# Performance work log

Measured on AMD Instinct MI355X. Metric: run time of the kernel, lower is better.

The kernel has to match this reference:

```python
import jax, jax.numpy as jnp
import numpy as np

NUM_HEADS = 8
LN_EPS = 1e-5


def _layernorm(t, w, b):
    mu = t.mean(-1, keepdims=True)
    var = t.var(-1, keepdims=True)  # ddof=0, matches torch LayerNorm
    return (t - mu) * jax.lax.rsqrt(var + LN_EPS) * w + b


def setup_inputs() -> dict:
    key = jax.random.key(0)
    ks = jax.random.split(key, 5)
    B, C, H, W = 16, 384, 32, 32
    hidden = 4 * C
    s = 0.02
    return {
        "x": jax.random.normal(ks[0], (B, C, H, W), jnp.float32),
        "ln1_w": jnp.ones((C,), jnp.float32),
        "ln1_b": jnp.zeros((C,), jnp.float32),
        "qkv_w": s * jax.random.normal(ks[1], (3 * C, C), jnp.float32),
        "qkv_b": jnp.zeros((3 * C,), jnp.float32),
        "proj_w": s * jax.random.normal(ks[2], (C, C), jnp.float32),
        "proj_b": jnp.zeros((C,), jnp.float32),
        "ln2_w": jnp.ones((C,), jnp.float32),
        "ln2_b": jnp.zeros((C,), jnp.float32),
        "fc1_w": s * jax.random.normal(ks[3], (hidden, C), jnp.float32),
        "fc1_b": jnp.zeros((hidden,), jnp.float32),
        "fc2_w": s * jax.random.normal(ks[4], (C, hidden), jnp.float32),
        "fc2_b": jnp.zeros((C,), jnp.float32),
    }


def reference(x, ln1_w, ln1_b, qkv_w, qkv_b, proj_w, proj_b,
              ln2_w, ln2_b, fc1_w, fc1_b, fc2_w, fc2_b):
    B, C, H, W = x.shape
    N = H * W
    nh = NUM_HEADS
    hd = C // nh
    scale = hd ** (-0.5)

    xf = x.reshape(B, C, N).transpose(0, 2, 1)  # (B, N, C) tokens

    # --- pre-norm attention ---
    h1 = _layernorm(xf, ln1_w, ln1_b)
    qkv = h1 @ qkv_w.T + qkv_b                      # (B, N, 3C)
    qkv = qkv.reshape(B, N, 3, nh, hd).transpose(2, 0, 3, 1, 4)  # (3,B,h,N,d)
    q, k, v = qkv[0], qkv[1], qkv[2]
    attn = jax.nn.softmax(jnp.einsum('bhnd,bhmd->bhnm', q, k) * scale, axis=-1)
    out = jnp.einsum('bhnm,bhmd->bhnd', attn, v)    # (B,h,N,d)
    out = out.transpose(0, 2, 1, 3).reshape(B, N, C)
    out = out @ proj_w.T + proj_b
    xf = xf + out

    # --- pre-norm FFN (exact GELU, matching torch nn.GELU default) ---
    h2 = _layernorm(xf, ln2_w, ln2_b)
    f = jax.nn.gelu(h2 @ fc1_w.T + fc1_b, approximate=False)
    f = f @ fc2_w.T + fc2_b
    xf = xf + f

    return xf.transpose(0, 2, 1).reshape(B, C, H, W)
```

## Files before the change

kernel.cpp:

```cpp
#include <hip/hip_runtime.h>

typedef unsigned short u16;
using bf16x8 = __attribute__((ext_vector_type(8))) short;
using f32x4  = __attribute__((ext_vector_type(4))) float;
using f32x16 = __attribute__((ext_vector_type(16))) float;

#define DEV __device__ __forceinline__

constexpr int    NTOK = 16384;
constexpr size_t QKSZ = (size_t)16 * 8 * 1024 * 64;
constexpr float  ATTN_SCALE = 0.14433756729740645f;

DEV u16 f2bf(float x) {
  unsigned int u = __float_as_uint(x);
  u += 0x7fffu + ((u >> 16) & 1u);
  return (u16)(u >> 16);
}

DEV void async16(const u16* g, u16* l) {
  __builtin_amdgcn_global_load_lds(
      (const __attribute__((address_space(1))) unsigned int*)g,
      (__attribute__((address_space(3))) unsigned int*)l, 16, 0, 0);
}

DEV const bf16x8* lds_swz(const u16* base, int row, int bytecol) {
  int byte = row * 128 + bytecol;
  byte ^= (row & 7) << 4;
  return (const bf16x8*)((const char*)base + byte);
}

DEV f32x16 zero16() {
  f32x16 z;
#pragma unroll
  for (int i = 0; i < 16; ++i) z[i] = 0.f;
  return z;
}

DEV float gelu_f(float x) {
  float y = 0.7978845608028654f * (x + 0.044715f * x * x * x);
  float e = __expf(2.f * y);
  float t = 1.f - 2.f / (e + 1.f);
  return 0.5f * x * (1.f + t);
}

DEV void xcd_remap(int& bx, int& by) {
  int p = blockIdx.x + gridDim.x * blockIdx.y;
  int nxs = gridDim.x >> 3;
  int xcd = p & 7, q = p >> 3;
  bx = xcd * nxs + q % nxs;
  by = q / nxs;
}

__global__ void cvt_kernel(const float* __restrict__ qkvw, const float* __restrict__ qkvb,
                           const float* __restrict__ projw, const float* __restrict__ fc1w,
                           const float* __restrict__ fc2w,
                           u16* __restrict__ wqkvp, float* __restrict__ biasp,
                           u16* __restrict__ wproj, u16* __restrict__ wfc1,
                           u16* __restrict__ wfc2) {
  int i = blockIdx.x * 256 + threadIdx.x;
  if (i < 147456) {
    int p = i / 96, q = (i - p * 96) * 4;
    int which = p >> 9, h = (p >> 6) & 7, d = p & 63;
    ushort4 o{0, 0, 0, 0};
    if (d < 48) {
      float sc = which ? 1.f : ATTN_SCALE;
      float4 v = *(const float4*)(qkvw + (size_t)(which * 384 + h * 48 + d) * 384 + q);
      o = ushort4{f2bf(v.x * sc), f2bf(v.y * sc), f2bf(v.z * sc), f2bf(v.w * sc)};
    }
    *(ushort4*)(wqkvp + (size_t)p * 384 + q) = o;
  } else if (i < 479232) {
    const float* s; u16* d; int off;
    if (i < 184320)      { s = projw; d = wproj; off = i - 147456; }
    else if (i < 331776) { s = fc1w;  d = wfc1;  off = i - 184320; }
    else                 { s = fc2w;  d = wfc2;  off = i - 331776; }
    float4 v = *(const float4*)(s + (size_t)off * 4);
    *(ushort4*)(d + (size_t)off * 4) = ushort4{f2bf(v.x), f2bf(v.y), f2bf(v.z), f2bf(v.w)};
  } else if (i < 479616) {
    int qi = (i - 479232) * 4;
    float4 o;
    float* op = (float*)&o;
#pragma unroll
    for (int r = 0; r < 4; ++r) {
      int p = qi + r, which = p >> 9, h = (p >> 6) & 7, d = p & 63;
      op[r] = (d < 48) ? qkvb[which * 384 + h * 48 + d] * (which ? 1.f : ATTN_SCALE) : 0.f;
    }
    *(float4*)(biasp + qi) = o;
  }
}

__global__ __launch_bounds__(256) void ln_kernel(
    const float* __restrict__ in, const float* __restrict__ gw,
    const float* __restrict__ gb, u16* __restrict__ out) {
  __shared__ float tile[32][385];
  __shared__ float mu_s[32], rs_s[32];
  const int b = blockIdx.y;
  const int n0 = blockIdx.x * 32;
  const int t = threadIdx.x;
  const int j = t & 31, cb = t >> 5;
  const float* src = in + (size_t)b * 384 * 1024 + n0;
  for (int k = 0; k < 48; ++k) {
    int c = k * 8 + cb;
    tile[j][c] = src[(size_t)c * 1024 + j];
  }
  __syncthreads();
  const int jt = t >> 3, r = t & 7;
  float s = 0.f, ss = 0.f;
  for (int c = r; c < 384; c += 8) { float v = tile[jt][c]; s += v; ss += v * v; }
  s += __shfl_xor(s, 1); ss += __shfl_xor(ss, 1);
  s += __shfl_xor(s, 2); ss += __shfl_xor(ss, 2);
  s += __shfl_xor(s, 4); ss += __shfl_xor(ss, 4);
  const float mean = s * (1.f / 384.f);
  const float var  = ss * (1.f / 384.f) - mean * mean;
  if (r == 0) { mu_s[jt] = mean; rs_s[jt] = rsqrtf(var + 1e-5f); }
  __syncthreads();
  for (int q = t; q < 3072; q += 256) {
    int tok = q / 96, c4 = (q - tok * 96) * 4;
    float m = mu_s[tok], rv = rs_s[tok];
    float4 wv = *(const float4*)(gw + c4);
    float4 bv = *(const float4*)(gb + c4);
    u16* dst = out + (size_t)(b * 1024 + n0 + tok) * 384 + c4;
    ushort4 o{f2bf((tile[tok][c4 + 0] - m) * rv * wv.x + bv.x),
              f2bf((tile[tok][c4 + 1] - m) * rv * wv.y + bv.y),
              f2bf((tile[tok][c4 + 2] - m) * rv * wv.z + bv.z),
              f2bf((tile[tok][c4 + 3] - m) * rv * wv.w + bv.w)};
    *(ushort4*)dst = o;
  }
}

template<int EPI>
__global__ __launch_bounds__(512, 2) void gemm256_kernel(
    const u16* __restrict__ A, const u16* __restrict__ W,
    const float* __restrict__ bias, u16* __restrict__ outh, int K) {
  __shared__ u16 sA[2][8192], sB[2][8192];
  int bx, by; xcd_remap(bx, by);
  const int m0 = bx * 256, n0 = by * 256;
  const int tid = threadIdx.x;
  const int wv = tid >> 6, lane = tid & 63;
  const int wm = (wv >> 2) * 128, wn = (wv & 3) * 64;
  const int l16 = lane & 15, lg = lane >> 4;
  const int rsw = ((lg ^ (l16 & 3)) << 4);

  f32x4 acc[8][4];
#pragma unroll
  for (int i = 0; i < 8; ++i)
#pragma unroll
    for (int jj = 0; jj < 4; ++jj) acc[i][jj] = f32x4{0.f, 0.f, 0.f, 0.f};

  const int nk = K >> 5;
  auto stage = [&](int buf, int kt) {
    const u16* Ab = A + (size_t)m0 * K + kt * 32;
    const u16* Wb = W + (size_t)n0 * K + kt * 32;
#pragma unroll
    for (int j = 0; j < 2; ++j) {
      int cb = j * 512 + wv * 64;
      int c = cb + lane;
      int row = c >> 2, sl = (c & 3) ^ (row & 3);
      async16(Ab + (size_t)row * K + sl * 8, &sA[buf][cb * 8]);
      async16(Wb + (size_t)row * K + sl * 8, &sB[buf][cb * 8]);
    }
  };
  stage(0, 0);
  int buf = 0;
  for (int kt = 0; kt < nk; ++kt) {
    asm volatile("s_waitcnt vmcnt(0)" ::: "memory");
    __builtin_amdgcn_s_barrier();
    if (kt + 1 < nk) stage(buf ^ 1, kt + 1);
    bf16x8 av[8], bv[4];
#pragma unroll
    for (int f = 0; f < 4; ++f)
      bv[f] = *(const bf16x8*)((const char*)&sB[buf][0] + (wn + f * 16 + l16) * 64 + rsw);
#pragma unroll
    for (int f = 0; f < 8; ++f)
      av[f] = *(const bf16x8*)((const char*)&sA[buf][0] + (wm + f * 16 + l16) * 64 + rsw);
    __builtin_amdgcn_s_setprio(1);
#pragma unroll
    for (int mf = 0; mf < 8; ++mf)
#pragma unroll
      for (int nf = 0; nf < 4; ++nf)
        acc[mf][nf] = __builtin_amdgcn_mfma_f32_16x16x32_bf16(bv[nf], av[mf], acc[mf][nf], 0, 0, 0);
    __builtin_amdgcn_s_setprio(0);
    buf ^= 1;
  }

#pragma unroll
  for (int mf = 0; mf < 8; ++mf) {
    const int token = m0 + wm + mf * 16 + l16;
    const int b = token >> 10, nn = token & 1023;
#pragma unroll
    for (int nf = 0; nf < 4; ++nf) {
      const int col = n0 + wn + nf * 16 + lg * 4;
      f32x4 v = acc[mf][nf];
      float4 bb = *(const float4*)(bias + col);
      unsigned long long pk = 0;
      if constexpr (EPI == 0) {
#pragma unroll
        for (int rr = 0; rr < 4; ++rr)
          pk |= (unsigned long long)f2bf(v[rr] + ((const float*)&bb)[rr]) << (16 * rr);
        const int which = col >> 9, h = (col >> 6) & 7, d0 = col & 63;
        size_t idx = (size_t)which * QKSZ + (size_t)((b * 8 + h) * 1024 + nn) * 64 + d0;
        *(unsigned long long*)&outh[idx] = pk;
      } else {
#pragma unroll
        for (int rr = 0; rr < 4; ++rr)
          pk |= (unsigned long long)f2bf(gelu_f(v[rr] + ((const float*)&bb)[rr])) << (16 * rr);
        *(unsigned long long*)&outh[(size_t)token * 1536 + col] = pk;
      }
    }
  }
}

template<int EPI>
__global__ __launch_bounds__(256, 2) void gemm_kernel(
    const u16* __restrict__ A, const u16* __restrict__ W,
    const float* __restrict__ bias, float* __restrict__ outf,
    u16* __restrict__ outh, const float* __restrict__ resid, int K) {
  __shared__ u16 sA[2][8192], sB[2][8192];
  int bx, by; xcd_remap(bx, by);
  const int m0 = bx * 128;
  const int n0 = (EPI == 4 ? 1024 : 0) + by * 128;
  const int wv = threadIdx.x >> 6, lane = threadIdx.x & 63;
  const int wm = (wv >> 1) * 64, wn = (wv & 1) * 64;
  const int l16 = lane & 15, lg = lane >> 4;
  const int ksw = (l16 & 7) << 4;

  f32x4 acc[4][4];
#pragma unroll
  for (int i = 0; i < 4; ++i)
#pragma unroll
    for (int jj = 0; jj < 4; ++jj) acc[i][jj] = f32x4{0.f, 0.f, 0.f, 0.f};

  const int nk = K >> 6;
  auto stage = [&](int buf, int kt) {
    const u16* Ab = A + (size_t)m0 * K + kt * 64;
    const u16* Wb = W + (size_t)n0 * K + kt * 64;
#pragma unroll
    for (int j = 0; j < 4; ++j) {
      int cb = j * 256 + wv * 64;
      int c = cb + lane;
      int row = c >> 3, sl = (c & 7) ^ (row & 7);
      async16(Ab + (size_t)row * K + sl * 8, &sA[buf][cb * 8]);
      async16(Wb + (size_t)row * K + sl * 8, &sB[buf][cb * 8]);
    }
  };
  stage(0, 0);
  int buf = 0;
  for (int kt = 0; kt < nk; ++kt) {
    asm volatile("s_waitcnt vmcnt(0)" ::: "memory");
    __builtin_amdgcn_s_barrier();
    if (kt + 1 < nk) stage(buf ^ 1, kt + 1);
#pragma unroll
    for (int ks = 0; ks < 2; ++ks) {
      bf16x8 av[4], bv[4];
#pragma unroll
      for (int f = 0; f < 4; ++f) {
        int ra = wm + f * 16 + l16, rb = wn + f * 16 + l16;
        av[f] = *(const bf16x8*)((const char*)&sA[buf][0] + ra * 128 + ((ks * 64 + lg * 16) ^ ksw));
        bv[f] = *(const bf16x8*)((const char*)&sB[buf][0] + rb * 128 + ((ks * 64 + lg * 16) ^ ksw));
      }
      __builtin_amdgcn_s_setprio(1);
#pragma unroll
      for (int mf = 0; mf < 4; ++mf)
#pragma unroll
        for (int nf = 0; nf < 4; ++nf)
          acc[mf][nf] = __builtin_amdgcn_mfma_f32_16x16x32_bf16(av[mf], bv[nf], acc[mf][nf], 0, 0, 0);
      __builtin_amdgcn_s_setprio(0);
    }
    buf ^= 1;
  }

#pragma unroll
  for (int mf = 0; mf < 4; ++mf) {
    const int mm = m0 + wm + mf * 16 + lg * 4;
    const int b = mm >> 10, nn = mm & 1023;
#pragma unroll
    for (int nf = 0; nf < 4; ++nf) {
      const int col = n0 + wn + nf * 16 + l16;
      f32x4 v = acc[mf][nf];
      const float bs = bias[col];
      if constexpr (EPI == 4) {
        unsigned long long pk = 0;
#pragma unroll
        for (int rr = 0; rr < 4; ++rr)
          pk |= (unsigned long long)f2bf(v[rr] + bs) << (16 * rr);
        const int h = (col >> 6) & 7, d = col & 63;
        size_t idx = 2ull * QKSZ + (((size_t)((b * 8 + h) * 64 + d)) << 10) + nn;
        *(unsigned long long*)&outh[idx] = pk;
      } else {
        size_t idx = ((size_t)(b * 384 + col) << 10) + nn;
        float4 rr4 = *(const float4*)&resid[idx];
        float4 o{v[0] + bs + rr4.x, v[1] + bs + rr4.y, v[2] + bs + rr4.z, v[3] + bs + rr4.w};
        *(float4*)&outf[idx] = o;
      }
    }
  }
}

__global__ __launch_bounds__(256, 3) void attn_kernel(
    const u16* __restrict__ Qg, const u16* __restrict__ Kg,
    const u16* __restrict__ Vtg, u16* __restrict__ outp) {
  __shared__ u16 Ks[2][4096];
  __shared__ u16 Vs[2][4096];
  __shared__ u16 Qs[8192];
  const int orig = blockIdx.x;
  const int swz = (orig & 7) * 128 + (orig >> 3);
  const int bh = swz >> 3, qt = swz & 7;
  const int w = threadIdx.x >> 6, lane = threadIdx.x & 63;
  const int l31 = lane & 31, hi = lane >> 5;

  const u16* kbase = Kg + (size_t)bh * 65536;
  const u16* vbase = Vtg + (size_t)bh * 65536;

  auto stageKV = [&](int buf, int kv) {
#pragma unroll
    for (int i = 0; i < 2; ++i) {
      int cb = (i * 4 + w) * 64;
      int ck = cb + lane;
      int g  = ck ^ ((ck >> 3) & 7);
      async16(kbase + (size_t)kv * 4096 + g * 8, &Ks[buf][cb * 8]);
      async16(vbase + (size_t)(g >> 3) * 1024 + kv * 64 + (g & 7) * 8, &Vs[buf][cb * 8]);
    }
  };

  {
    const u16* src = Qg + (size_t)(bh * 1024 + qt * 128) * 64;
#pragma unroll
    for (int i = 0; i < 4; ++i) {
      int cb = (i * 4 + w) * 64;
      int ck = cb + lane;
      int g  = ck ^ ((ck >> 3) & 7);
      async16(src + g * 8, &Qs[cb * 8]);
    }
  }
  stageKV(0, 0);
  asm volatile("s_waitcnt vmcnt(0)" ::: "memory");
  __builtin_amdgcn_s_barrier();

  bf16x8 qf[4];
#pragma unroll
  for (int ds = 0; ds < 4; ++ds)
    qf[ds] = *lds_swz(Qs, w * 32 + l31, ds * 32 + hi * 16);

  f32x16 out0 = zero16(), out1 = zero16();
  float ls0 = 0.f, ls1 = 0.f;

  int buf = 0;
  for (int kv = 0; kv < 16; ++kv) {
    if (kv + 1 < 16) stageKV(buf ^ 1, kv + 1);

    f32x16 sacc0 = zero16(), sacc1 = zero16();
    __builtin_amdgcn_s_setprio(1);
#pragma unroll
    for (int ds = 0; ds < 4; ++ds) {
      bf16x8 kf0 = *lds_swz(Ks[buf], l31,      ds * 32 + hi * 16);
      bf16x8 kf1 = *lds_swz(Ks[buf], 32 + l31, ds * 32 + hi * 16);
      sacc0 = __builtin_amdgcn_mfma_f32_32x32x16_bf16(kf0, qf[ds], sacc0, 0, 0, 0);
      sacc1 = __builtin_amdgcn_mfma_f32_32x32x16_bf16(kf1, qf[ds], sacc1, 0, 0, 0);
    }
    __builtin_amdgcn_s_setprio(0);

    unsigned int c0[8], c1[8];
#pragma unroll
    for (int i = 0; i < 8; ++i) {
      float a = __expf(sacc0[2 * i]), b = __expf(sacc0[2 * i + 1]);
      ls0 += a + b;
      unsigned int pk;
      asm("v_cvt_pk_bf16_f32 %0, %1, %2" : "=v"(pk) : "v"(a), "v"(b));
      c0[i] = pk;
    }
#pragma unroll
    for (int i = 0; i < 8; ++i) {
      float a = __expf(sacc1[2 * i]), b = __expf(sacc1[2 * i + 1]);
      ls1 += a + b;
      unsigned int pk;
      asm("v_cvt_pk_bf16_f32 %0, %1, %2" : "=v"(pk) : "v"(a), "v"(b));
      c1[i] = pk;
    }

#pragma unroll
    for (int m = 0; m < 4; ++m) {
      unsigned int a0 = (m < 2) ? c0[(m & 1) * 4 + 0] : c1[(m & 1) * 4 + 0];
      unsigned int b0 = (m < 2) ? c0[(m & 1) * 4 + 2] : c1[(m & 1) * 4 + 2];
      unsigned int a1 = (m < 2) ? c0[(m & 1) * 4 + 1] : c1[(m & 1) * 4 + 1];
      unsigned int b1 = (m < 2) ? c0[(m & 1) * 4 + 3] : c1[(m & 1) * 4 + 3];
      asm volatile("v_permlane32_swap_b32 %0, %1" : "+v"(a0), "+v"(b0));
      asm volatile("v_permlane32_swap_b32 %0, %1" : "+v"(a1), "+v"(b1));
      union { int4 i; bf16x8 v; } u;
      u.i = int4{(int)a0, (int)a1, (int)b0, (int)b1};
      bf16x8 pa = u.v;
      bf16x8 v0 = *lds_swz(Vs[buf], l31,      m * 32 + hi * 16);
      bf16x8 v1 = *lds_swz(Vs[buf], 32 + l31, m * 32 + hi * 16);
      __builtin_amdgcn_s_setprio(1);
      out0 = __builtin_amdgcn_mfma_f32_32x32x16_bf16(pa, v0, out0, 0, 0, 0);
      out1 = __builtin_amdgcn_mfma_f32_32x32x16_bf16(pa, v1, out1, 0, 0, 0);
      __builtin_amdgcn_s_setprio(0);
    }

    asm volatile("s_waitcnt vmcnt(0)" ::: "memory");
    __builtin_amdgcn_s_barrier();
    buf ^= 1;
  }

  float lf = ls0 + ls1;
  lf += __shfl_xor(lf, 32);
  const int b = bh >> 3, h = bh & 7;
#pragma unroll
  for (int r = 0; r < 16; ++r) {
    const int q = (r & 3) + 8 * (r >> 2) + 4 * hi;
    const float inv = 1.f / __shfl(lf, q);
    const int token = qt * 128 + w * 32 + q;
    const size_t rowb = (size_t)(b * 1024 + token) * 384 + h * 48;
    outp[rowb + l31] = f2bf(out0[r] * inv);
    if (l31 < 16) outp[rowb + 32 + l31] = f2bf(out1[r] * inv);
  }
}

constexpr size_t OFF_WQKVP = 0;
constexpr size_t OFF_BIASP = 1179648;
constexpr size_t OFF_WPROJ = 1185792;
constexpr size_t OFF_WFC1  = 1480704;
constexpr size_t OFF_WFC2  = 2660352;
constexpr size_t OFF_H     = 3840000;
constexpr size_t OFF_QKV   = 16422912;
constexpr size_t OFF_AO    = 66754560;
constexpr size_t OFF_Y1T   = 79337472;

extern "C" void kernel_launch(void* const* d_in, const int* in_sizes, int n_in,
                              void* d_out, int out_size, void* d_ws, size_t ws_size,
                              hipStream_t stream) {
  (void)in_sizes; (void)n_in; (void)out_size; (void)ws_size;
  const float* x     = (const float*)d_in[0];
  const float* ln1w  = (const float*)d_in[1];
  const float* ln1b  = (const float*)d_in[2];
  const float* qkvw  = (const float*)d_in[3];
  const float* qkvbi = (const float*)d_in[4];
  const float* projw = (const float*)d_in[5];
  const float* projb = (const float*)d_in[6];
  const float* ln2w  = (const float*)d_in[7];
  const float* ln2b  = (const float*)d_in[8];
  const float* fc1w  = (const float*)d_in[9];
  const float* fc1b  = (const float*)d_in[10];
  const float* fc2w  = (const float*)d_in[11];
  const float* fc2b  = (const float*)d_in[12];

  char* ws = (char*)d_ws;
  u16*   wqkvp = (u16*)(ws + OFF_WQKVP);
  float* biasp = (float*)(ws + OFF_BIASP);
  u16*   wproj = (u16*)(ws + OFF_WPROJ);
  u16*   wfc1  = (u16*)(ws + OFF_WFC1);
  u16*   wfc2  = (u16*)(ws + OFF_WFC2);
  u16*   h1    = (u16*)(ws + OFF_H);
  u16*   qkvs  = (u16*)(ws + OFF_QKV);
  u16*   f1    = qkvs;
  u16*   ao    = (u16*)(ws + OFF_AO);
  float* y1t   = (float*)(ws + OFF_Y1T);

  cvt_kernel<<<1874, 256, 0, stream>>>(qkvw, qkvbi, projw, fc1w, fc2w,
                                       wqkvp, biasp, wproj, wfc1, wfc2);

  dim3 lngrid(32, 16);
  ln_kernel<<<lngrid, 256, 0, stream>>>(x, ln1w, ln1b, h1);

  gemm256_kernel<0><<<dim3(64, 4), 512, 0, stream>>>(h1, wqkvp, biasp, qkvs, 384);
  gemm_kernel<4><<<dim3(128, 4), 256, 0, stream>>>(h1, wqkvp, biasp, nullptr, qkvs, nullptr, 384);

  attn_kernel<<<dim3(1024), 256, 0, stream>>>(qkvs, qkvs + QKSZ, qkvs + 2 * QKSZ, ao);

  gemm_kernel<1><<<dim3(128, 3), 256, 0, stream>>>(ao, wproj, projb, y1t, nullptr, x, 384);

  ln_kernel<<<lngrid, 256, 0, stream>>>(y1t, ln2w, ln2b, h1 );

  gemm256_kernel<2><<<dim3(64, 6), 512, 0, stream>>>(h1, wfc1, fc1b, f1, 384);

  gemm_kernel<3><<<dim3(128, 3), 256, 0, stream>>>(f1, wfc2, fc2b, (float*)d_out, nullptr, y1t, 1536);
}
```

Before: 315.0 us.

## Unify GEMMs into one 128x128 K32 kernel with swapped-operand epilogues

Replaces the 256x256 512-thread GEMM and the 128x128 K64 GEMM with a single 128x128 tile, K-step 32 kernel at occupancy 4. For some epilogues it swaps the MFMA operand order so each lane holds consecutive columns or consecutive tokens. Stores become scalar 16-bit or 32-bit writes instead of packed 64-bit or float4 writes. The aim is more blocks and higher occupancy with half the LDS, paid for with less data reuse per tile, more global loads, and narrower, less coalesced output stores.

```diff
diff --git a/kernel.cpp b/kernel.cpp
--- a/kernel.cpp
+++ b/kernel.cpp
@@ -128,21 +128,23 @@
 }
 
 template<int EPI>
-__global__ __launch_bounds__(512, 2) void gemm256_kernel(
+__global__ __launch_bounds__(256, 4) void gemm_kernel(
     const u16* __restrict__ A, const u16* __restrict__ W,
-    const float* __restrict__ bias, u16* __restrict__ outh, int K) {
-  __shared__ u16 sA[2][8192], sB[2][8192];
+    const float* __restrict__ bias, float* __restrict__ outf,
+    u16* __restrict__ outh, const float* __restrict__ resid, int K) {
+  constexpr bool SWAP = (EPI == 1 || EPI == 3 || EPI == 4);
+  __shared__ u16 sA[2][4096], sB[2][4096];
   int bx, by; xcd_remap(bx, by);
-  const int m0 = bx * 256, n0 = by * 256;
-  const int tid = threadIdx.x;
-  const int wv = tid >> 6, lane = tid & 63;
-  const int wm = (wv >> 2) * 128, wn = (wv & 3) * 64;
+  const int m0 = bx * 128;
+  const int n0 = (EPI == 4 ? 1024 : 0) + by * 128;
+  const int wv = threadIdx.x >> 6, lane = threadIdx.x & 63;
+  const int wm = (wv >> 1) * 64, wn = (wv & 1) * 64;
   const int l16 = lane & 15, lg = lane >> 4;
-  const int rsw = ((lg ^ (l16 & 3)) << 4);
-
-  f32x4 acc[8][4];
-#pragma unroll
-  for (int i = 0; i < 8; ++i)
+  const int rsw = (lg ^ (l16 & 3)) << 4;
+
+  f32x4 acc[4][4];
+#pragma unroll
+  for (int i = 0; i < 4; ++i)
 #pragma unroll
     for (int jj = 0; jj < 4; ++jj) acc[i][jj] = f32x4{0.f, 0.f, 0.f, 0.f};
 
@@ -151,8 +153,8 @@
     const u16* Ab = A + (size_t)m0 * K + kt * 32;
     const u16* Wb = W + (size_t)n0 * K + kt * 32;
 #pragma unroll
-    for (int j = 0; j < 2; ++j) {
-      int cb = j * 512 + wv * 64;
+    for (int i = 0; i < 2; ++i) {
+      int cb = i * 256 + wv * 64;
       int c = cb + lane;
       int row = c >> 2, sl = (c & 3) ^ (row & 3);
       async16(Ab + (size_t)row * K + sl * 8, &sA[buf][cb * 8]);
@@ -165,131 +167,73 @@
     asm volatile("s_waitcnt vmcnt(0)" ::: "memory");
     __builtin_amdgcn_s_barrier();
     if (kt + 1 < nk) stage(buf ^ 1, kt + 1);
-    bf16x8 av[8], bv[4];
-#pragma unroll
-    for (int f = 0; f < 4; ++f)
+    bf16x8 av[4], bv[4];
+#pragma unroll
+    for (int f = 0; f < 4; ++f) {
+      av[f] = *(const bf16x8*)((const char*)&sA[buf][0] + (wm + f * 16 + l16) * 64 + rsw);
       bv[f] = *(const bf16x8*)((const char*)&sB[buf][0] + (wn + f * 16 + l16) * 64 + rsw);
-#pragma unroll
-    for (int f = 0; f < 8; ++f)
-      av[f] = *(const bf16x8*)((const char*)&sA[buf][0] + (wm + f * 16 + l16) * 64 + rsw);
+    }
     __builtin_amdgcn_s_setprio(1);
 #pragma unroll
-    for (int mf = 0; mf < 8; ++mf)
-#pragma unroll
-      for (int nf = 0; nf < 4; ++nf)
-        acc[mf][nf] = __builtin_amdgcn_mfma_f32_16x16x32_bf16(bv[nf], av[mf], acc[mf][nf], 0, 0, 0);
+    for (int mf = 0; mf < 4; ++mf)
+#pragma unroll
+      for (int nf = 0; nf < 4; ++nf) {
+        if constexpr (SWAP)
+          acc[mf][nf] = __builtin_amdgcn_mfma_f32_16x16x32_bf16(bv[nf], av[mf], acc[mf][nf], 0, 0, 0);
+        else
+          acc[mf][nf] = __builtin_amdgcn_mfma_f32_16x16x32_bf16(av[mf], bv[nf], acc[mf][nf], 0, 0, 0);
+      }
     __builtin_amdgcn_s_setprio(0);
     buf ^= 1;
   }
 
-#pragma unroll
-  for (int mf = 0; mf < 8; ++mf) {
-    const int token = m0 + wm + mf * 16 + l16;
-    const int b = token >> 10, nn = token & 1023;
-#pragma unroll
-    for (int nf = 0; nf < 4; ++nf) {
-      const int col = n0 + wn + nf * 16 + lg * 4;
-      f32x4 v = acc[mf][nf];
-      float4 bb = *(const float4*)(bias + col);
-      unsigned long long pk = 0;
-      if constexpr (EPI == 0) {
-#pragma unroll
-        for (int rr = 0; rr < 4; ++rr)
-          pk |= (unsigned long long)f2bf(v[rr] + ((const float*)&bb)[rr]) << (16 * rr);
-        const int which = col >> 9, h = (col >> 6) & 7, d0 = col & 63;
-        size_t idx = (size_t)which * QKSZ + (size_t)((b * 8 + h) * 1024 + nn) * 64 + d0;
-        *(unsigned long long*)&outh[idx] = pk;
-      } else {
-#pragma unroll
-        for (int rr = 0; rr < 4; ++rr)
-          pk |= (unsigned long long)f2bf(gelu_f(v[rr] + ((const float*)&bb)[rr])) << (16 * rr);
-        *(unsigned long long*)&outh[(size_t)token * 1536 + col] = pk;
+  if constexpr (!SWAP) {
+#pragma unroll
+    for (int mf = 0; mf < 4; ++mf) {
+      const int mm = m0 + wm + mf * 16 + lg * 4;
+      const int b = mm >> 10, nnb = mm & 1023;
+#pragma unroll
+      for (int nf = 0; nf < 4; ++nf) {
+        const int col = n0 + wn + nf * 16 + l16;
+        f32x4 v = acc[mf][nf];
+        const float bs = bias[col];
+        if constexpr (EPI == 0) {
+          const int which = col >> 9, h = (col >> 6) & 7, d0 = col & 63;
+          size_t base = (size_t)which * QKSZ + (((size_t)(b * 8 + h)) << 16) + (size_t)nnb * 64 + d0;
+#pragma unroll
+          for (int rr = 0; rr < 4; ++rr) outh[base + (size_t)rr * 64] = f2bf(v[rr] + bs);
+        } else {
+#pragma unroll
+          for (int rr = 0; rr < 4; ++rr)
+            outh[(size_t)(mm + rr) * 1536 + col] = f2bf(gelu_f(v[rr] + bs));
+        }
       }
     }
-  }
-}
-
-template<int EPI>
-__global__ __launch_bounds__(256, 2) void gemm_kernel(
-    const u16* __restrict__ A, const u16* __restrict__ W,
-    const float* __restrict__ bias, float* __restrict__ outf,
-    u16* __restrict__ outh, const float* __restrict__ resid, int K) {
-  __shared__ u16 sA[2][8192], sB[2][8192];
-  int bx, by; xcd_remap(bx, by);
-  const int m0 = bx * 128;
-  const int n0 = (EPI == 4 ? 1024 : 0) + by * 128;
-  const int wv = threadIdx.x >> 6, lane = threadIdx.x & 63;
-  const int wm = (wv >> 1) * 64, wn = (wv & 1) * 64;
-  const int l16 = lane & 15, lg = lane >> 4;
-  const int ksw = (l16 & 7) << 4;
-
-  f32x4 acc[4][4];
-#pragma unroll
-  for (int i = 0; i < 4; ++i)
-#pragma unroll
-    for (int jj = 0; jj < 4; ++jj) acc[i][jj] = f32x4{0.f, 0.f, 0.f, 0.f};
-
-  const int nk = K >> 6;
-  auto stage = [&](int buf, int kt) {
-    const u16* Ab = A + (size_t)m0 * K + kt * 64;
-    const u16* Wb = W + (size_t)n0 * K + kt * 64;
-#pragma unroll
-    for (int j = 0; j < 4; ++j) {
-      int cb = j * 256 + wv * 64;
-      int c = cb + lane;
-      int row = c >> 3, sl = (c & 7) ^ (row & 7);
-      async16(Ab + (size_t)row * K + sl * 8, &sA[buf][cb * 8]);
-      async16(Wb + (size_t)row * K + sl * 8, &sB[buf][cb * 8]);
-    }
-  };
-  stage(0, 0);
-  int buf = 0;
-  for (int kt = 0; kt < nk; ++kt) {
-    asm volatile("s_waitcnt vmcnt(0)" ::: "memory");
-    __builtin_amdgcn_s_barrier();
-    if (kt + 1 < nk) stage(buf ^ 1, kt + 1);
-#pragma unroll
-    for (int ks = 0; ks < 2; ++ks) {
-      bf16x8 av[4], bv[4];
-#pragma unroll
-      for (int f = 0; f < 4; ++f) {
-        int ra = wm + f * 16 + l16, rb = wn + f * 16 + l16;
-        av[f] = *(const bf16x8*)((const char*)&sA[buf][0] + ra * 128 + ((ks * 64 + lg * 16) ^ ksw));
-        bv[f] = *(const bf16x8*)((const char*)&sB[buf][0] + rb * 128 + ((ks * 64 + lg * 16) ^ ksw));
-      }
-      __builtin_amdgcn_s_setprio(1);
-#pragma unroll
-      for (int mf = 0; mf < 4; ++mf)
-#pragma unroll
-        for (int nf = 0; nf < 4; ++nf)
-          acc[mf][nf] = __builtin_amdgcn_mfma_f32_16x16x32_bf16(av[mf], bv[nf], acc[mf][nf], 0, 0, 0);
-      __builtin_amdgcn_s_setprio(0);
-    }
-    buf ^= 1;
-  }
-
-#pragma unroll
-  for (int mf = 0; mf < 4; ++mf) {
-    const int mm = m0 + wm + mf * 16 + lg * 4;
-    const int b = mm >> 10, nn = mm & 1023;
-#pragma unroll
-    for (int nf = 0; nf < 4; ++nf) {
-      const int col = n0 + wn + nf * 16 + l16;
-      f32x4 v = acc[mf][nf];
-      const float bs = bias[col];
-      if constexpr (EPI == 4) {
-        unsigned long long pk = 0;
-#pragma unroll
-        for (int rr = 0; rr < 4; ++rr)
-          pk |= (unsigned long long)f2bf(v[rr] + bs) << (16 * rr);
-        const int h = (col >> 6) & 7, d = col & 63;
-        size_t idx = 2ull * QKSZ + (((size_t)((b * 8 + h) * 64 + d)) << 10) + nn;
-        *(unsigned long long*)&outh[idx] = pk;
-      } else {
-        size_t idx = ((size_t)(b * 384 + col) << 10) + nn;
-        float4 rr4 = *(const float4*)&resid[idx];
-        float4 o{v[0] + bs + rr4.x, v[1] + bs + rr4.y, v[2] + bs + rr4.z, v[3] + bs + rr4.w};
-        *(float4*)&outf[idx] = o;
+  } else {
+#pragma unroll
+    for (int mf = 0; mf < 4; ++mf) {
+      const int token = m0 + wm + mf * 16 + l16;
+      const int b = token >> 10, nn = token & 1023;
+#pragma unroll
+      for (int nf = 0; nf < 4; ++nf) {
+        const int colb = n0 + wn + nf * 16 + lg * 4;
+        f32x4 v = acc[mf][nf];
+        float4 bb = *(const float4*)(bias + colb);
+        if constexpr (EPI == 4) {
+#pragma unroll
+          for (int rr = 0; rr < 4; ++rr) {
+            const int col = colb + rr, h = (col >> 6) & 7, d = col & 63;
+            outh[2ull * QKSZ + (((size_t)((b * 8 + h) * 64 + d)) << 10) + nn] =
+                f2bf(v[rr] + ((const float*)&bb)[rr]);
+          }
+        } else {
+#pragma unroll
+          for (int rr = 0; rr < 4; ++rr) {
+            const int col = colb + rr;
+            size_t idx = (((size_t)(b * 384 + col)) << 10) + nn;
+            outf[idx] = v[rr] + ((const float*)&bb)[rr] + resid[idx];
+          }
+        }
       }
     }
   }
@@ -460,7 +404,7 @@
   dim3 lngrid(32, 16);
   ln_kernel<<<lngrid, 256, 0, stream>>>(x, ln1w, ln1b, h1);
 
-  gemm256_kernel<0><<<dim3(64, 4), 512, 0, stream>>>(h1, wqkvp, biasp, qkvs, 384);
+  gemm_kernel<0><<<dim3(128, 8), 256, 0, stream>>>(h1, wqkvp, biasp, nullptr, qkvs, nullptr, 384);
   gemm_kernel<4><<<dim3(128, 4), 256, 0, stream>>>(h1, wqkvp, biasp, nullptr, qkvs, nullptr, 384);
 
   attn_kernel<<<dim3(1024), 256, 0, stream>>>(qkvs, qkvs + QKSZ, qkvs + 2 * QKSZ, ao);
@@ -469,7 +413,7 @@
 
   ln_kernel<<<lngrid, 256, 0, stream>>>(y1t, ln2w, ln2b, h1 );
 
-  gemm256_kernel<2><<<dim3(64, 6), 512, 0, stream>>>(h1, wfc1, fc1b, f1, 384);
+  gemm_kernel<2><<<dim3(128, 12), 256, 0, stream>>>(h1, wfc1, fc1b, nullptr, f1, nullptr, 384);
 
   gemm_kernel<3><<<dim3(128, 3), 256, 0, stream>>>(f1, wfc2, fc2b, (float*)d_out, nullptr, y1t, 1536);
 }
```

New measurement: 314.2 us. No clear change (-0.2%).
